# Kernel optimization log

Hardware: AMD Instinct MI355X
Metric: run time of the kernel (lower is better)

## Reference

```python
import jax, jax.numpy as jnp
import numpy as np

HO, WO = 64, 64
SHARPNESS = 150.0


def _stereographic_grid(ho, wo):
    # Matches create_normal_grid(..., 'stereographic'); torch.meshgrid 'ij':
    # v varies over rows (ho), u over cols (wo).
    v, u = np.meshgrid(np.arange(ho), np.arange(wo), indexing='ij')
    p = 4.0 * ((u + 0.5) / wo - 0.5)
    q = -4.0 * ((v + 0.5) / ho - 0.5)
    d = 1.0 + p ** 2 + q ** 2
    z = -(-1.0 + p ** 2 + q ** 2) / d
    m = (z > 0.0).astype(np.float32)
    x = 2.0 * p / d * m
    y = 2.0 * q / d * m
    z = z * m
    return np.stack([x, y, z], axis=-1).reshape(-1, 3).astype(np.float32)  # [ho*wo,3]


_GRID = _stereographic_grid(HO, WO)
_IDX = np.nonzero(np.any(_GRID != 0, axis=-1))[0]  # static valid-query indices [N]
_QN = _GRID[_IDX]  # [N,3]


def setup_inputs() -> dict:
    key = jax.random.key(0)
    k1, k2, k3 = jax.random.split(key, 3)
    bs, c, h, w = 2, 64, 192, 192
    in_fea_map = jax.random.normal(k1, (bs, c, h, w), dtype=jnp.float32)
    nrm = jax.random.normal(k2, (bs, 3, h, w), dtype=jnp.float32)
    in_normal_map = nrm / (jnp.linalg.norm(nrm, axis=1, keepdims=True) + 1e-8)
    in_mask_map = (jax.random.uniform(k3, (bs, 1, h, w)) > 0.2).astype(jnp.float32)
    log_query_norm = jnp.full((1,), np.log(SHARPNESS), dtype=jnp.float32)
    return {"in_fea_map": in_fea_map, "in_normal_map": in_normal_map,
            "in_mask_map": in_mask_map, "log_query_norm": log_query_norm}


def reference(in_fea_map, in_normal_map, in_mask_map, log_query_norm):
    bs, c, h, w = in_fea_map.shape
    hw = h * w
    qn = jnp.asarray(_QN, dtype=in_fea_map.dtype)  # [N,3] static valid queries
    vals = in_fea_map.reshape(bs, c, hw).transpose(0, 2, 1)       # [bs,HW,c]
    key_n = in_normal_map.reshape(bs, 3, hw)                       # [bs,3,HW]
    cos = jnp.einsum('nd,bdm->bnm', qn, key_n)                     # [bs,N,HW]
    dps = cos / np.float32(np.sqrt(3.0))
    dps = dps - jnp.max(dps, axis=-1, keepdims=True)
    w_ = jnp.exp(jnp.exp(log_query_norm) * dps)                    # dropout in eval = identity
    w_ = w_ * in_mask_map.reshape(bs, 1, hw)
    weights = w_ / (jnp.sum(w_, axis=-1, keepdims=True) + 1e-9)    # [bs,N,HW]
    mapped = weights @ vals                                        # [bs,N,c]
    mapped = jnp.concatenate([jnp.broadcast_to(qn, (bs,) + qn.shape), mapped], axis=-1)
    # variance map over last 3 feature channels
    mean = mapped[..., -3:]
    sq_mean = weights @ (vals[..., -3:] ** 2)
    var = jnp.sum(sq_mean - mean ** 2, axis=-1, keepdims=True)
    mapped = jnp.concatenate([var, mapped], axis=-1)
    # cosine map
    rm_cos = jnp.sum(weights * cos, axis=-1, keepdims=True)
    mapped = jnp.concatenate([rm_cos, mapped], axis=-1)            # [bs,N,c+5]
    C = mapped.shape[-1]
    out = jnp.zeros((bs, HO * WO, C), mapped.dtype).at[:, _IDX, :].set(mapped)
    return out.transpose(0, 2, 1).reshape(bs, C, HO, WO)
```

## Files before the change

kernel.cpp:

```cpp
#include <hip/hip_runtime.h>
#include <hip/hip_bf16.h>
#include <cstdint>
#include <cstddef>

#define HW 36864
#define QT 64
#define NCHA 69
#define NCHK 576

constexpr bool is_valid_px(int v, int u) {
  int a = 2 * u - 63, b = 2 * v - 63;
  return a * a + b * b < 1024;
}
constexpr int count_valid() {
  int n = 0;
  for (int v = 0; v < 64; ++v)
    for (int u = 0; u < 64; ++u)
      if (is_valid_px(v, u)) ++n;
  return n;
}
constexpr int NV  = count_valid();
constexpr int NQT = (NV + QT - 1) / QT;
constexpr int NQP = NQT * QT;
constexpr int PLANE = 2 * NQP * NCHA;

constexpr size_t BM_SHORTS  = (size_t)2 * NCHK * 80 * 64;
constexpr size_t BM_BYTES   = BM_SHORTS * 2;
constexpr size_t NV_BYTES   = (size_t)2 * HW * 4 * 4;
constexpr size_t PART_OFF   = BM_BYTES + NV_BYTES;

struct QTab {
  short idx[NQP];
  short rank[4096];
};
constexpr QTab make_qtab() {
  QTab t{};
  int n = 0;
  for (int p = 0; p < 4096; ++p) {
    int v = p >> 6, u = p & 63;
    if (is_valid_px(v, u)) { t.idx[n] = (short)p; t.rank[p] = (short)n; ++n; }
    else t.rank[p] = -1;
  }
  for (int i = n; i < NQP; ++i) t.idx[i] = -1;
  return t;
}
__constant__ QTab g_qtab = make_qtab();

typedef short short8 __attribute__((ext_vector_type(8)));
typedef float f32x4  __attribute__((ext_vector_type(4)));

__device__ __forceinline__ ushort2 f2b2(float a, float b) {
  __hip_bfloat162 h = __float22bfloat162_rn(make_float2(a, b));
  return *(ushort2*)&h;
}
__device__ __forceinline__ void pix2qn(int pix, float& x, float& y, float& z) {
  x = 0.f; y = 0.f; z = 0.f;
  if (pix >= 0) {
    int v = pix >> 6, u = pix & 63;
    float p = (float)(2 * u - 63) * (1.0f / 32.0f);
    float q = -(float)(2 * v - 63) * (1.0f / 32.0f);
    float d = 1.0f + p * p + q * q;
    x = 2.0f * p / d; y = 2.0f * q / d; z = (1.0f - p * p - q * q) / d;
  }
}

#define PREP_BM_BLKS 2880
#define PREP_NV_BLKS 288
#define PREP_ZF_BLKS 224
#define PREP_BLKS (PREP_BM_BLKS + PREP_NV_BLKS + PREP_ZF_BLKS)

__global__ __launch_bounds__(256) void prep_kernel(
    const float* __restrict__ fea,
    const float* __restrict__ nrm,
    const float* __restrict__ msk,
    const float* __restrict__ lqn,
    unsigned short* __restrict__ Bm,
    float* __restrict__ nv,
    float* __restrict__ out)
{
  const float Cc = __expf(lqn[0]) * 0.57735026919f;
  if (blockIdx.x < PREP_BM_BLKS) {
    int gid = blockIdx.x * 256 + threadIdx.x;
    int g   = gid & 7;
    int row = (gid >> 3) % 80;
    int chk = ((gid >> 3) / 80) % NCHK;
    int b   = gid / (8 * 80 * NCHK);
    int px0 = chk * 64 + g * 8;
    float v[8];
    if (row < 64) {
      const float* p = fea + ((size_t)b * 64 + row) * HW + px0;
      #pragma unroll
      for (int i = 0; i < 8; ++i) v[i] = p[i];
    } else if (row < 67) {
      const float* p = fea + ((size_t)b * 64 + (61 + row - 64)) * HW + px0;
      #pragma unroll
      for (int i = 0; i < 8; ++i) { float x = p[i]; v[i] = x * x; }
    } else if (row < 70) {
      const float* p = nrm + ((size_t)b * 3 + (row - 67)) * HW + px0;
      #pragma unroll
      for (int i = 0; i < 8; ++i) v[i] = p[i];
    } else {
      float c = (row == 70) ? 1.0f : 0.0f;
      #pragma unroll
      for (int i = 0; i < 8; ++i) v[i] = c;
    }
    short8 o;
    #pragma unroll
    for (int p2 = 0; p2 < 4; ++p2) {
      ushort2 pr = f2b2(v[2 * p2], v[2 * p2 + 1]);
      o[2 * p2] = (short)pr.x; o[2 * p2 + 1] = (short)pr.y;
    }
    *(short8*)&Bm[(((size_t)b * NCHK + chk) * 80 + row) * 64 + g * 8] = o;
  } else if (blockIdx.x < PREP_BM_BLKS + PREP_NV_BLKS) {
    int p = (blockIdx.x - PREP_BM_BLKS) * 256 + threadIdx.x;
    int b = p / HW, px = p % HW;
    float nx = nrm[((size_t)b * 3 + 0) * HW + px];
    float ny = nrm[((size_t)b * 3 + 1) * HW + px];
    float nz = nrm[((size_t)b * 3 + 2) * HW + px];
    float mk = msk[(size_t)b * HW + px];
    float bias = -Cc + (mk > 0.5f ? 0.f : -2000.f);
    *(float4*)&nv[(size_t)p * 4] = make_float4(Cc * nx, Cc * ny, Cc * nz, bias);
  } else {
    const int start = (blockIdx.x - PREP_BM_BLKS - PREP_NV_BLKS) * 256 + threadIdx.x;
    const int strd  = PREP_ZF_BLKS * 256;
    const int TOT   = 2 * NCHA * 4096;
    for (int i = start; i < TOT; i += strd) {
      if (g_qtab.rank[i & 4095] < 0) out[i] = 0.0f;
    }
  }
}

template<int KSC>
__global__ __launch_bounds__(256, 4) void partial_kernel(
    const unsigned short* __restrict__ Bm,
    const float* __restrict__ nv,
    float* __restrict__ part)
{
  constexpr int SLICE  = HW / KSC;
  constexpr int NCHUNK = SLICE / 64;

  __shared__ __align__(16) unsigned short v_s[2][80][72];
  __shared__ __align__(16) float nrm4_s[2][64][4];

  const int bx  = blockIdx.x;
  const int cls = bx & 7;
  const int r0  = bx >> 3;
  const int qt  = r0 % NQT;
  const int sh  = r0 / NQT;
  const int s   = sh * 8 + cls;
  const int b   = s / KSC;
  const int ks  = s % KSC;

  const int t    = threadIdx.x;
  const int wv   = t >> 6;
  const int Mh   = wv & 1;
  const int kko  = (wv >> 1) * 32;
  const int l    = t & 63;
  const int lq   = l >> 4;
  const int mrow = l & 15;

  float qx[2], qy[2], qz[2];
  pix2qn(g_qtab.idx[qt * QT + 32 * Mh + mrow],      qx[0], qy[0], qz[0]);
  pix2qn(g_qtab.idx[qt * QT + 32 * Mh + 16 + mrow], qx[1], qy[1], qz[1]);

  const int g0r = t >> 3,          g0c = (t & 7) * 8;
  const int g1r = (t + 256) >> 3;
  const int g2r = (t + 512) >> 3;
  const int pxp = 32 * (l >> 5) + 4 * (l & 7) + ((l >> 3) & 3);

  f32x4 acc[2][5];
  #pragma unroll
  for (int h = 0; h < 2; ++h)
    #pragma unroll
    for (int nt = 0; nt < 5; ++nt) acc[h][nt] = (f32x4)(0.0f);

  short8 pB[3];
  float4 pnv;

  auto load_chunk = [&](int ck) {
    int chkAbs = ks * NCHUNK + ck;
    const unsigned short* src = Bm + ((size_t)b * NCHK + chkAbs) * (80 * 64);
    pB[0] = *(const short8*)(src + (size_t)(t)       * 8);
    pB[1] = *(const short8*)(src + (size_t)(t + 256) * 8);
    if (t < 128) pB[2] = *(const short8*)(src + (size_t)(t + 512) * 8);
    if (t < 64)  pnv = *(const float4*)&nv[((size_t)b * HW + chkAbs * 64 + l) * 4];
  };
  auto store_chunk = [&](int buf) {
    *(short8*)&v_s[buf][g0r][g0c] = pB[0];
    *(short8*)&v_s[buf][g1r][g0c] = pB[1];
    if (t < 128) *(short8*)&v_s[buf][g2r][g0c] = pB[2];
    if (t < 64)  *(float4*)&nrm4_s[buf][pxp][0] = pnv;
  };

  load_chunk(0);
  store_chunk(0);
  __syncthreads();

  for (int ck = 0; ck < NCHUNK; ++ck) {
    const int buf = ck & 1;
    if (ck + 1 < NCHUNK) load_chunk(ck + 1);

    float e0[8], e1[8];
    #pragma unroll
    for (int j = 0; j < 8; ++j) {
      const float4 nvv = *(const float4*)&nrm4_s[buf][kko + 4 * j + lq][0];
      float t0 = fmaf(qx[0], nvv.x, fmaf(qy[0], nvv.y, fmaf(qz[0], nvv.z, nvv.w)));
      float t1 = fmaf(qx[1], nvv.x, fmaf(qy[1], nvv.y, fmaf(qz[1], nvv.z, nvv.w)));
      e0[j] = __expf(t0);
      e1[j] = __expf(t1);
    }
    short8 a0, a1;
    #pragma unroll
    for (int p = 0; p < 4; ++p) {
      ushort2 p0 = f2b2(e0[2 * p], e0[2 * p + 1]);
      ushort2 p1 = f2b2(e1[2 * p], e1[2 * p + 1]);
      a0[2 * p] = (short)p0.x; a0[2 * p + 1] = (short)p0.y;
      a1[2 * p] = (short)p1.x; a1[2 * p + 1] = (short)p1.y;
    }
    #pragma unroll
    for (int nt = 0; nt < 5; ++nt) {
      short8 bb = *(const short8*)&v_s[buf][16 * nt + mrow][kko + 8 * lq];
      acc[0][nt] = __builtin_amdgcn_mfma_f32_16x16x32_bf16(a0, bb, acc[0][nt], 0, 0, 0);
      acc[1][nt] = __builtin_amdgcn_mfma_f32_16x16x32_bf16(a1, bb, acc[1][nt], 0, 0, 0);
    }

    if (ck + 1 < NCHUNK) {
      store_chunk(buf ^ 1);
      __syncthreads();
    }
  }

  __syncthreads();
  float* scr = (float*)&v_s[0][0][0];
  float* exs = scr + 64 * 80;

  if (kko) {
    #pragma unroll
    for (int h = 0; h < 2; ++h)
      #pragma unroll
      for (int nt = 0; nt < 5; ++nt)
        #pragma unroll
        for (int rr = 0; rr < 4; ++rr) {
          int qloc = 32 * Mh + 16 * h + 4 * lq + rr;
          scr[qloc * 80 + 16 * nt + mrow] = acc[h][nt][rr];
        }
  }
  __syncthreads();
  const size_t pbase = (size_t)ks * PLANE + ((size_t)b * NQP + (size_t)(qt * QT)) * NCHA;
  if (!kko) {
    #pragma unroll
    for (int h = 0; h < 2; ++h) {
      #pragma unroll
      for (int nt = 0; nt < 5; ++nt)
        #pragma unroll
        for (int rr = 0; rr < 4; ++rr) {
          int qloc = 32 * Mh + 16 * h + 4 * lq + rr;
          acc[h][nt][rr] += scr[qloc * 80 + 16 * nt + mrow];
        }
      #pragma unroll
      for (int nt = 0; nt < 4; ++nt)
        #pragma unroll
        for (int rr = 0; rr < 4; ++rr) {
          int qloc = 32 * Mh + 16 * h + 4 * lq + rr;
          part[pbase + (size_t)qloc * NCHA + (size_t)(16 * nt + mrow)] = acc[h][nt][rr];
        }
      if (mrow < 7) {
        #pragma unroll
        for (int rr = 0; rr < 4; ++rr)
          exs[(32 * Mh + 16 * h + 4 * lq + rr) * 9 + mrow] = acc[h][4][rr];
      }
    }
  }
  __syncthreads();
  if (t < 64) {
    float gx, gy, gz;
    pix2qn(g_qtab.idx[qt * QT + t], gx, gy, gz);
    const float* E = exs + t * 9;
    float swc = gx * E[3] + gy * E[4] + gz * E[5];
    size_t o = pbase + (size_t)t * NCHA;
    part[o + 64] = E[0];
    part[o + 65] = E[1];
    part[o + 66] = E[2];
    part[o + 67] = swc;
    part[o + 68] = E[6];
  }
}

#define NFIN (2 * NQT * 8)

__global__ __launch_bounds__(256) void finalize_kernel(
    const float* __restrict__ part,
    float* __restrict__ out,
    int ksc)
{
  const int blk = blockIdx.x;
  const int t   = threadIdx.x;

  __shared__ float sm[8][NCHA];
  const int b   = blk / (NQT * 8);
  const int rem = blk % (NQT * 8);
  const int qt  = rem >> 3;
  const int qr  = rem & 7;
  const int q0  = qt * QT + qr * 8;

  const size_t colbase = ((size_t)b * NQP + (size_t)q0) * NCHA;
  for (int i = t; i < 8 * NCHA; i += 256) {
    float sv = 0.f;
    const size_t off = colbase + (size_t)i;
    #pragma unroll 8
    for (int k = 0; k < ksc; ++k) sv += part[(size_t)k * PLANE + off];
    sm[0][i] = sv;
  }
  __syncthreads();

  for (int i = t; i < 8 * NCHA; i += 256) {
    const int ql = i / NCHA;
    const int oc = i % NCHA;
    const int pix = g_qtab.idx[q0 + ql];
    if (pix < 0) continue;
    const float* A = sm[ql];
    const float inv = 1.0f / (A[68] + 1e-9f);
    float gx, gy, gz;
    pix2qn(pix, gx, gy, gz);
    float val;
    if (oc == 0)      val = A[67] * inv;
    else if (oc == 1) {
      val = 0.f;
      #pragma unroll
      for (int j = 0; j < 3; ++j) {
        float m  = A[61 + j] * inv;
        float sq = A[64 + j] * inv;
        val += sq - m * m;
      }
    }
    else if (oc == 2) val = gx;
    else if (oc == 3) val = gy;
    else if (oc == 4) val = gz;
    else              val = A[oc - 5] * inv;
    out[((size_t)b * NCHA + (size_t)oc) * 4096 + pix] = val;
  }
}

extern "C" void kernel_launch(void* const* d_in, const int* in_sizes, int n_in,
                              void* d_out, int out_size, void* d_ws, size_t ws_size,
                              hipStream_t stream) {
  const float* fea = (const float*)d_in[0];
  const float* nrm = (const float*)d_in[1];
  const float* msk = (const float*)d_in[2];
  const float* lqn = (const float*)d_in[3];
  unsigned short* Bm = (unsigned short*)d_ws;
  float* nv   = (float*)((char*)d_ws + BM_BYTES);
  float* part = (float*)((char*)d_ws + PART_OFF);
  float* out  = (float*)d_out;

  prep_kernel<<<dim3(PREP_BLKS), 256, 0, stream>>>(fea, nrm, msk, lqn, Bm, nv, out);

  const size_t need64 = PART_OFF + (size_t)PLANE * 64 * sizeof(float);
  const size_t need32 = PART_OFF + (size_t)PLANE * 32 * sizeof(float);
  if (ws_size >= need64) {
    partial_kernel<64><<<dim3(2 * 64 * NQT), 256, 0, stream>>>(Bm, nv, part);
    finalize_kernel<<<dim3(NFIN), 256, 0, stream>>>(part, out, 64);
  } else if (ws_size >= need32) {
    partial_kernel<32><<<dim3(2 * 32 * NQT), 256, 0, stream>>>(Bm, nv, part);
    finalize_kernel<<<dim3(NFIN), 256, 0, stream>>>(part, out, 32);
  } else {
    partial_kernel<16><<<dim3(2 * 16 * NQT), 256, 0, stream>>>(Bm, nv, part);
    finalize_kernel<<<dim3(NFIN), 256, 0, stream>>>(part, out, 16);
  }
}
```

Baseline: 117.9 us.

## Stream B and normal chunks into LDS via global_load_lds DMA

The prep kernel now writes the bf16 B chunks with a padded 72-element row stride and stores the normal/bias vectors already permuted into the LDS order. The partial kernel then copies each chunk straight from global memory into LDS with `__builtin_amdgcn_global_load_lds`, instead of loading into registers and storing to LDS itself. This is meant to remove the register staging and the separate LDS store phase, and to cut VGPR pressure in the main loop. In exchange, prep writes about 9/8 as much B data, because of the zero padding. Correctness now depends on the barrier waiting for the asynchronous LDS writes to finish.

```diff
diff --git a/kernel.cpp b/kernel.cpp
--- a/kernel.cpp
+++ b/kernel.cpp
@@ -24,9 +24,9 @@
 constexpr int NQP = NQT * QT;
 constexpr int PLANE = 2 * NQP * NCHA;
 
-constexpr size_t BM_SHORTS  = (size_t)2 * NCHK * 80 * 64;
-constexpr size_t BM_BYTES   = BM_SHORTS * 2;
-constexpr size_t NV_BYTES   = (size_t)2 * HW * 4 * 4;
+constexpr size_t BM_CHUNK_B = (size_t)80 * 72 * 2;
+constexpr size_t BM_BYTES   = (size_t)2 * NCHK * BM_CHUNK_B;
+constexpr size_t NV_BYTES   = (size_t)2 * NCHK * 64 * 16;
 constexpr size_t PART_OFF   = BM_BYTES + NV_BYTES;
 
 struct QTab {
@@ -48,6 +48,8 @@
 
 typedef short short8 __attribute__((ext_vector_type(8)));
 typedef float f32x4  __attribute__((ext_vector_type(4)));
+typedef const __attribute__((address_space(1))) void g_void;
+typedef __attribute__((address_space(3))) void l_void;
 
 __device__ __forceinline__ ushort2 f2b2(float a, float b) {
   __hip_bfloat162 h = __float22bfloat162_rn(make_float2(a, b));
@@ -64,7 +66,7 @@
   }
 }
 
-#define PREP_BM_BLKS 2880
+#define PREP_BM_BLKS 3240
 #define PREP_NV_BLKS 288
 #define PREP_ZF_BLKS 224
 #define PREP_BLKS (PREP_BM_BLKS + PREP_NV_BLKS + PREP_ZF_BLKS)
@@ -81,28 +83,33 @@
   const float Cc = __expf(lqn[0]) * 0.57735026919f;
   if (blockIdx.x < PREP_BM_BLKS) {
     int gid = blockIdx.x * 256 + threadIdx.x;
-    int g   = gid & 7;
-    int row = (gid >> 3) % 80;
-    int chk = ((gid >> 3) / 80) % NCHK;
-    int b   = gid / (8 * 80 * NCHK);
-    int px0 = chk * 64 + g * 8;
+    int g   = gid % 9;
+    int row = (gid / 9) % 80;
+    int chk = ((gid / 9) / 80) % NCHK;
+    int b   = gid / (9 * 80 * NCHK);
     float v[8];
-    if (row < 64) {
-      const float* p = fea + ((size_t)b * 64 + row) * HW + px0;
-      #pragma unroll
-      for (int i = 0; i < 8; ++i) v[i] = p[i];
-    } else if (row < 67) {
-      const float* p = fea + ((size_t)b * 64 + (61 + row - 64)) * HW + px0;
-      #pragma unroll
-      for (int i = 0; i < 8; ++i) { float x = p[i]; v[i] = x * x; }
-    } else if (row < 70) {
-      const float* p = nrm + ((size_t)b * 3 + (row - 67)) * HW + px0;
-      #pragma unroll
-      for (int i = 0; i < 8; ++i) v[i] = p[i];
+    if (g == 8) {
+      #pragma unroll
+      for (int i = 0; i < 8; ++i) v[i] = 0.f;
     } else {
-      float c = (row == 70) ? 1.0f : 0.0f;
-      #pragma unroll
-      for (int i = 0; i < 8; ++i) v[i] = c;
+      int px0 = chk * 64 + g * 8;
+      if (row < 64) {
+        const float* p = fea + ((size_t)b * 64 + row) * HW + px0;
+        #pragma unroll
+        for (int i = 0; i < 8; ++i) v[i] = p[i];
+      } else if (row < 67) {
+        const float* p = fea + ((size_t)b * 64 + (61 + row - 64)) * HW + px0;
+        #pragma unroll
+        for (int i = 0; i < 8; ++i) { float x = p[i]; v[i] = x * x; }
+      } else if (row < 70) {
+        const float* p = nrm + ((size_t)b * 3 + (row - 67)) * HW + px0;
+        #pragma unroll
+        for (int i = 0; i < 8; ++i) v[i] = p[i];
+      } else {
+        float c = (row == 70) ? 1.0f : 0.0f;
+        #pragma unroll
+        for (int i = 0; i < 8; ++i) v[i] = c;
+      }
     }
     short8 o;
     #pragma unroll
@@ -110,16 +117,19 @@
       ushort2 pr = f2b2(v[2 * p2], v[2 * p2 + 1]);
       o[2 * p2] = (short)pr.x; o[2 * p2 + 1] = (short)pr.y;
     }
-    *(short8*)&Bm[(((size_t)b * NCHK + chk) * 80 + row) * 64 + g * 8] = o;
+    *(short8*)&Bm[(((size_t)b * NCHK + chk) * 80 + row) * 72 + g * 8] = o;
   } else if (blockIdx.x < PREP_BM_BLKS + PREP_NV_BLKS) {
     int p = (blockIdx.x - PREP_BM_BLKS) * 256 + threadIdx.x;
     int b = p / HW, px = p % HW;
+    int chk = px >> 6, l = px & 63;
+    int pxp = 32 * (l >> 5) + 4 * (l & 7) + ((l >> 3) & 3);
     float nx = nrm[((size_t)b * 3 + 0) * HW + px];
     float ny = nrm[((size_t)b * 3 + 1) * HW + px];
     float nz = nrm[((size_t)b * 3 + 2) * HW + px];
     float mk = msk[(size_t)b * HW + px];
     float bias = -Cc + (mk > 0.5f ? 0.f : -2000.f);
-    *(float4*)&nv[(size_t)p * 4] = make_float4(Cc * nx, Cc * ny, Cc * nz, bias);
+    *(float4*)&nv[(((size_t)b * NCHK + chk) * 64 + pxp) * 4]
+        = make_float4(Cc * nx, Cc * ny, Cc * nz, bias);
   } else {
     const int start = (blockIdx.x - PREP_BM_BLKS - PREP_NV_BLKS) * 256 + threadIdx.x;
     const int strd  = PREP_ZF_BLKS * 256;
@@ -163,42 +173,41 @@
   pix2qn(g_qtab.idx[qt * QT + 32 * Mh + mrow],      qx[0], qy[0], qz[0]);
   pix2qn(g_qtab.idx[qt * QT + 32 * Mh + 16 + mrow], qx[1], qy[1], qz[1]);
 
-  const int g0r = t >> 3,          g0c = (t & 7) * 8;
-  const int g1r = (t + 256) >> 3;
-  const int g2r = (t + 512) >> 3;
-  const int pxp = 32 * (l >> 5) + 4 * (l & 7) + ((l >> 3) & 3);
-
   f32x4 acc[2][5];
   #pragma unroll
   for (int h = 0; h < 2; ++h)
     #pragma unroll
     for (int nt = 0; nt < 5; ++nt) acc[h][nt] = (f32x4)(0.0f);
 
-  short8 pB[3];
-  float4 pnv;
-
-  auto load_chunk = [&](int ck) {
+  auto issue_dma = [&](int ck, int buf) {
     int chkAbs = ks * NCHUNK + ck;
-    const unsigned short* src = Bm + ((size_t)b * NCHK + chkAbs) * (80 * 64);
-    pB[0] = *(const short8*)(src + (size_t)(t)       * 8);
-    pB[1] = *(const short8*)(src + (size_t)(t + 256) * 8);
-    if (t < 128) pB[2] = *(const short8*)(src + (size_t)(t + 512) * 8);
-    if (t < 64)  pnv = *(const float4*)&nv[((size_t)b * HW + chkAbs * 64 + l) * 4];
+    const char* srcB = (const char*)Bm + ((size_t)b * NCHK + chkAbs) * BM_CHUNK_B;
+    char* dstB = (char*)&v_s[buf][0][0];
+    #pragma unroll
+    for (int i = 0; i < 3; ++i) {
+      int seg = wv + 4 * i;
+      if (seg < 11)
+        __builtin_amdgcn_global_load_lds(
+            (g_void*)(srcB + (size_t)seg * 1024 + (size_t)l * 16),
+            (l_void*)(dstB + (size_t)seg * 1024), 16, 0, 0);
+    }
+    if (wv == 3) {
+      __builtin_amdgcn_global_load_lds(
+          (g_void*)(srcB + (size_t)11 * 1024 + (size_t)l * 4),
+          (l_void*)(dstB + (size_t)11 * 1024), 4, 0, 0);
+      const char* srcN = (const char*)nv + (((size_t)b * NCHK + chkAbs) * 64) * 16;
+      __builtin_amdgcn_global_load_lds(
+          (g_void*)(srcN + (size_t)l * 16),
+          (l_void*)&nrm4_s[buf][0][0], 16, 0, 0);
+    }
   };
-  auto store_chunk = [&](int buf) {
-    *(short8*)&v_s[buf][g0r][g0c] = pB[0];
-    *(short8*)&v_s[buf][g1r][g0c] = pB[1];
-    if (t < 128) *(short8*)&v_s[buf][g2r][g0c] = pB[2];
-    if (t < 64)  *(float4*)&nrm4_s[buf][pxp][0] = pnv;
-  };
-
-  load_chunk(0);
-  store_chunk(0);
+
+  issue_dma(0, 0);
   __syncthreads();
 
   for (int ck = 0; ck < NCHUNK; ++ck) {
     const int buf = ck & 1;
-    if (ck + 1 < NCHUNK) load_chunk(ck + 1);
+    if (ck + 1 < NCHUNK) issue_dma(ck + 1, buf ^ 1);
 
     float e0[8], e1[8];
     #pragma unroll
@@ -224,10 +233,7 @@
       acc[1][nt] = __builtin_amdgcn_mfma_f32_16x16x32_bf16(a1, bb, acc[1][nt], 0, 0, 0);
     }
 
-    if (ck + 1 < NCHUNK) {
-      store_chunk(buf ^ 1);
-      __syncthreads();
-    }
+    if (ck + 1 < NCHUNK) __syncthreads();
   }
 
   __syncthreads();
```

New measurement: 118.4 us. About the same (+0.4%).
